# Optimization experiments

Measured on AMD Instinct MI355X. Metric: run time of the kernel, lower is better.

Reference implementation:

```python
import jax, jax.numpy as jnp
import numpy as np
from jax import lax

B, N, C = 8, 8192, 91          # batch, num_boxes, num_classes (incl. background)
CM = C - 1                      # foreground classes
K = 1000                        # pre_nms_num_detections (per-class candidates / max per class)
MAX_TOTAL = 100                 # post_nms_num_detections
IOU_THR = 0.3
SCORE_THR = 0.0
BBOX_W = (10.0, 10.0, 5.0, 5.0)
BBOX_CLIP = float(np.log(1000.0 / 16.0))
IMG = 1024.0


def setup_inputs() -> dict:
    key = jax.random.key(0)
    k1, k2, k3, k4, k5, k6 = jax.random.split(key, 6)
    class_outputs = jax.random.normal(k1, (B, N, C), jnp.float32)
    box_outputs = jax.random.normal(k2, (B, N, C * 4), jnp.float32)
    cy = jax.random.uniform(k3, (B, N), minval=0.0, maxval=IMG)
    cx = jax.random.uniform(k4, (B, N), minval=0.0, maxval=IMG)
    sh = jax.random.uniform(k5, (B, N), minval=16.0, maxval=256.0)
    sw = jax.random.uniform(k6, (B, N), minval=16.0, maxval=256.0)
    anchor_boxes = jnp.stack([
        jnp.clip(cy - 0.5 * sh, 0.0, IMG), jnp.clip(cx - 0.5 * sw, 0.0, IMG),
        jnp.clip(cy + 0.5 * sh, 0.0, IMG), jnp.clip(cx + 0.5 * sw, 0.0, IMG)], axis=-1)
    image_info = jnp.tile(jnp.array([IMG, IMG, 1.0, 1.0], jnp.float32), (B, 1))
    return {"class_outputs": class_outputs, "box_outputs": box_outputs,
            "anchor_boxes": anchor_boxes, "image_info": image_info}


def decode_boxes(enc, anchors):
    # enc, anchors: [..., 4] (ty,tx,th,tw) / (ymin,xmin,ymax,xmax)
    wy, wx, wh, ww = BBOX_W
    ah = anchors[..., 2] - anchors[..., 0]
    aw = anchors[..., 3] - anchors[..., 1]
    acy = anchors[..., 0] + 0.5 * ah
    acx = anchors[..., 1] + 0.5 * aw
    ty = enc[..., 0] / wy
    tx = enc[..., 1] / wx
    th = jnp.minimum(enc[..., 2] / wh, BBOX_CLIP)
    tw = jnp.minimum(enc[..., 3] / ww, BBOX_CLIP)
    cy = ty * ah + acy
    cx = tx * aw + acx
    h = jnp.exp(th) * ah
    w = jnp.exp(tw) * aw
    return jnp.stack([cy - 0.5 * h, cx - 0.5 * w, cy + 0.5 * h, cx + 0.5 * w], axis=-1)


def pairwise_iou(b):  # b: [K,4] -> [K,K]
    area = jnp.maximum(b[:, 2] - b[:, 0], 0.0) * jnp.maximum(b[:, 3] - b[:, 1], 0.0)
    ih = jnp.maximum(jnp.minimum(b[:, None, 2], b[None, :, 2]) - jnp.maximum(b[:, None, 0], b[None, :, 0]), 0.0)
    iw = jnp.maximum(jnp.minimum(b[:, None, 3], b[None, :, 3]) - jnp.maximum(b[:, None, 1], b[None, :, 1]), 0.0)
    inter = ih * iw
    return inter / (area[:, None] + area[None, :] - inter + 1e-8)


def _per_class_nms(bc, sc):
    # bc: [N,4] normalized boxes, sc: [N] scores -> (kept boxes [K,4], scores [K], suppressed -> -1)
    sk, idx = lax.top_k(sc, K)
    bk = bc[idx]
    overlap = pairwise_iou(bk) > IOU_THR   # bool [K,K], sorted by score desc
    pass_thr = sk > SCORE_THR
    def body(i, keep):
        sup = jnp.any(keep & overlap[:, i])
        return keep.at[i].set(pass_thr[i] & jnp.logical_not(sup))
    keep = lax.fori_loop(0, K, body, jnp.zeros((K,), jnp.bool_))
    return bk, jnp.where(keep, sk, -1.0)


def _per_image(norm_boxes, sc):
    # norm_boxes: [N,CM,4], sc: [N,CM]
    bks, sks = jax.vmap(_per_class_nms)(jnp.transpose(norm_boxes, (1, 0, 2)), sc.T)
    fs = sks.reshape(-1)          # [CM*K]
    fb = bks.reshape(-1, 4)
    ts, ti = lax.top_k(fs, MAX_TOTAL)
    tb = fb[ti]
    tc = (ti // K).astype(jnp.float32)   # 0-based fg class index
    valid = ts > SCORE_THR
    ts = jnp.where(valid, ts, 0.0)
    tb = jnp.where(valid[:, None], tb, 0.0)
    tc = jnp.where(valid, tc, 0.0)
    return tb, ts, tc, jnp.sum(valid).astype(jnp.int32)


def reference(class_outputs, box_outputs, anchor_boxes, image_info):
    probs = jax.nn.softmax(class_outputs, axis=-1)
    scores = probs[..., 1:]                                   # [B,N,CM]
    enc = box_outputs.reshape(B, N, C, 4)[:, :, 1:, :]        # [B,N,CM,4]
    anchors = jnp.broadcast_to(anchor_boxes[:, :, None, :], (B, N, CM, 4))
    boxes = decode_boxes(enc, anchors)                        # [B,N,CM,4]
    h = image_info[:, 0]
    w = image_info[:, 1]
    hw = jnp.stack([h, w, h, w], axis=-1)                     # [B,4]
    boxes = jnp.clip(boxes, 0.0, hw[:, None, None, :])        # clip to image
    norm_boxes = boxes / hw[:, None, None, :]                 # to_normalized_coordinates
    pb, ps, pc, nv = lax.map(lambda a: _per_image(*a), (norm_boxes, scores))
    post_boxes = pb * hw[:, None, :]                          # to_absolute_coordinates
    post_classes = pc + 1.0                                   # shift back over background
    return (nv, post_boxes, post_classes, ps)
```

## Files before the change

### kernel.cpp

```cpp
#include <hip/hip_runtime.h>
#include <math.h>

#define Bb 8
#define Nn 8192
#define Cc 91
#define CM 90
#define Kk 1000
#define MAXT 100
#define KSEL 256
#define NW 4
#define IOU_THR 0.3f
#define BBOX_CLIP 4.135166556742356f
#define IMG 1024.0f
#define SM_ROWS 64

typedef unsigned long long u64;
typedef unsigned int u32;

__global__ __launch_bounds__(64) void softmax_scores(
    const float* __restrict__ cls, float* __restrict__ scores_t) {
    __shared__ float rowbuf[SM_ROWS * Cc];
    int blk = blockIdx.x;
    int lane = threadIdx.x;
    const float4* src = (const float4*)(cls + (size_t)blk * SM_ROWS * Cc);
    for (int i = lane; i < SM_ROWS * Cc / 4; i += 64) {
        float4 v = src[i];
        *(float4*)&rowbuf[i * 4] = v;
    }
    __syncthreads();
    int row_g = blk * SM_ROWS + lane;
    int b = row_g >> 13;
    int n = row_g & (Nn - 1);
    float* row = &rowbuf[lane * Cc];
    float m = row[0];
    for (int c = 1; c < Cc; c++) m = fmaxf(m, row[c]);
    float s = 0.0f;
    for (int c = 0; c < Cc; c++) {
        float e = expf(row[c] - m);
        row[c] = e;
        s += e;
    }
    for (int c = 1; c < Cc; c++) {
        float p = row[c] / s;
        scores_t[((size_t)(b * CM + (c - 1))) * Nn + n] = p;
    }
}

__global__ __launch_bounds__(512) void topk_nms(
    const float* __restrict__ scores_t,
    const float* __restrict__ box_out, const float* __restrict__ anchors,
    u64* __restrict__ cand_key, float* __restrict__ cand_box) {
    __shared__ __align__(16) char smem[21264];
    int* hist1 = (int*)smem;
    int* hist2 = (int*)(smem + 4096);
    u64* keys  = (u64*)(smem + 8192);
    int* eqidx = (int*)(smem + 10240);
    u64* keys2 = (u64*)(smem + 11264);
    float* dy1 = (float*)(smem + 13312);
    float* dx1 = (float*)(smem + 14336);
    float* dy2 = (float*)(smem + 15360);
    float* dx2 = (float*)(smem + 16384);
    float* dar = (float*)(smem + 17408);
    float4* kb = (float4*)(smem + 18432);
    float* kar = (float*)(smem + 20032);
    u64* kkey  = (u64*)(smem + 20432);
    int* scal  = (int*)(smem + 21232);
    #define sh_need  scal[0]
    #define sh_digit scal[1]
    #define sh_cnt   scal[2]
    #define sh_eq    scal[3]
    #define sh_kcnt  scal[4]

    int bc = blockIdx.x;
    int b = bc / CM;
    int c = bc % CM;
    int tid = threadIdx.x;
    int wave = tid >> 6, lane = tid & 63;

    hist1[tid] = 0; hist1[tid + 512] = 0;
    hist2[tid] = 0; hist2[tid + 512] = 0;
    if (tid == 0) { sh_need = KSEL; sh_cnt = 0; sh_eq = 0; }
    __syncthreads();

    const float4* s4 = (const float4*)(scores_t + (size_t)bc * Nn);
    float4 v0 = s4[tid];
    float4 v1 = s4[tid + 512];
    float4 v2 = s4[tid + 1024];
    float4 v3 = s4[tid + 1536];
    u32 x[16];
    x[0]  = __float_as_uint(v0.x); x[1]  = __float_as_uint(v0.y);
    x[2]  = __float_as_uint(v0.z); x[3]  = __float_as_uint(v0.w);
    x[4]  = __float_as_uint(v1.x); x[5]  = __float_as_uint(v1.y);
    x[6]  = __float_as_uint(v1.z); x[7]  = __float_as_uint(v1.w);
    x[8]  = __float_as_uint(v2.x); x[9]  = __float_as_uint(v2.y);
    x[10] = __float_as_uint(v2.z); x[11] = __float_as_uint(v2.w);
    x[12] = __float_as_uint(v3.x); x[13] = __float_as_uint(v3.y);
    x[14] = __float_as_uint(v3.z); x[15] = __float_as_uint(v3.w);
    #pragma unroll
    for (int k = 0; k < 16; k++) atomicAdd(&hist1[x[k] >> 20], 1);
    __syncthreads();

    #define SELECT_DIGIT(H)                                                  \
    {                                                                        \
        int4 h0 = *(const int4*)&(H)[16 * lane];                             \
        int4 h1 = *(const int4*)&(H)[16 * lane + 4];                         \
        int4 h2 = *(const int4*)&(H)[16 * lane + 8];                         \
        int4 h3 = *(const int4*)&(H)[16 * lane + 12];                        \
        int cnt[16] = {h0.x, h0.y, h0.z, h0.w, h1.x, h1.y, h1.z, h1.w,       \
                       h2.x, h2.y, h2.z, h2.w, h3.x, h3.y, h3.z, h3.w};      \
        int gsum = 0;                                                        \
        _Pragma("unroll")                                                    \
        for (int j = 0; j < 16; j++) gsum += cnt[j];                         \
        int run = gsum;                                                      \
        for (int off = 1; off < 64; off <<= 1) {                             \
            int vv = __shfl_down(run, off, 64);                              \
            if (lane + off < 64) run += vv;                                  \
        }                                                                    \
        int sa = run - gsum;                                                 \
        int need = sh_need;                                                  \
        if (need > sa && need <= sa + gsum) {                                \
            int acc = sa;                                                    \
            _Pragma("unroll")                                                \
            for (int j = 15; j >= 0; j--) {                                  \
                if (acc + cnt[j] >= need) {                                  \
                    sh_digit = 16 * lane + j;                                \
                    sh_need = need - acc;                                    \
                    break;                                                   \
                }                                                            \
                acc += cnt[j];                                               \
            }                                                                \
        }                                                                    \
    }

    if (wave == 0) SELECT_DIGIT(hist1);
    __syncthreads();
    u32 P12 = (u32)sh_digit;

    #pragma unroll
    for (int k = 0; k < 16; k++)
        if ((x[k] >> 20) == P12) atomicAdd(&hist2[(x[k] >> 10) & 1023], 1);
    __syncthreads();

    if (wave == 0) { SELECT_DIGIT(hist2); }
    else { for (int i = tid - 64; i < 1024; i += 448) hist1[i] = 0; }
    __syncthreads();
    u32 P22 = (P12 << 10) | (u32)sh_digit;

    #pragma unroll
    for (int k = 0; k < 16; k++)
        if ((x[k] >> 10) == P22) atomicAdd(&hist1[x[k] & 1023], 1);
    __syncthreads();

    if (wave == 0) SELECT_DIGIT(hist1);
    __syncthreads();
    u32 Tb = (P22 << 10) | (u32)sh_digit;
    int m = sh_need;
    #undef SELECT_DIGIT

    #pragma unroll
    for (int k = 0; k < 16; k++) {
        u32 v = x[k];
        int idx = ((k >> 2) << 11) + (tid << 2) + (k & 3);
        if (v > Tb) {
            int pp = atomicAdd(&sh_cnt, 1);
            keys[pp] = ((u64)v << 13) | (u64)(8191 - idx);
        } else if (v == Tb) {
            int pp = atomicAdd(&sh_eq, 1);
            if (pp < 256) eqidx[pp] = idx;
        }
    }
    __syncthreads();
    if (tid == 0) {
        int e = min(sh_eq, 256);
        for (int t = 0; t < m; t++) {
            int best = -1, bi = 0x7FFFFFFF;
            for (int q = 0; q < e; q++) {
                int ii = eqidx[q];
                if (ii < bi) { bi = ii; best = q; }
            }
            if (best >= 0) {
                eqidx[best] = 0x7FFFFFFF;
                int pp = atomicAdd(&sh_cnt, 1);
                keys[pp] = ((u64)Tb << 13) | (u64)(8191 - bi);
            }
        }
    }
    __syncthreads();

    if (tid < KSEL) {
        u64 my = keys[tid];
        int n = 8191 - (int)(my & 0x1FFF);
        const float4 e = *(const float4*)(box_out + ((size_t)(b * Nn + n)) * (Cc * 4) + (size_t)(c + 1) * 4);
        const float4 a = *(const float4*)(anchors + (size_t)(b * Nn + n) * 4);
        int r = 0;
        #pragma unroll 8
        for (int q = 0; q < KSEL; q++) r += (keys[q] > my) ? 1 : 0;
        keys2[r] = my;
        float ah = a.z - a.x, aw = a.w - a.y;
        float acy = a.x + 0.5f * ah, acx = a.y + 0.5f * aw;
        float ty = e.x / 10.0f, tx = e.y / 10.0f;
        float th = fminf(e.z / 5.0f, BBOX_CLIP);
        float tw = fminf(e.w / 5.0f, BBOX_CLIP);
        float cy = ty * ah + acy, cx = tx * aw + acx;
        float h = expf(th) * ah, w = expf(tw) * aw;
        float y1 = cy - 0.5f * h, x1 = cx - 0.5f * w;
        float y2 = cy + 0.5f * h, x2 = cx + 0.5f * w;
        y1 = fminf(fmaxf(y1, 0.0f), IMG) * (1.0f / IMG);
        x1 = fminf(fmaxf(x1, 0.0f), IMG) * (1.0f / IMG);
        y2 = fminf(fmaxf(y2, 0.0f), IMG) * (1.0f / IMG);
        x2 = fminf(fmaxf(x2, 0.0f), IMG) * (1.0f / IMG);
        float area = fmaxf(y2 - y1, 0.0f) * fmaxf(x2 - x1, 0.0f);
        dy1[r] = y1; dx1[r] = x1;
        dy2[r] = y2; dx2[r] = x2;
        dar[r] = area;
    }
    __syncthreads();

    if (tid < 64) {
        int kcnt = 0;
        for (int ci = 0; ci < NW && kcnt < MAXT; ci++) {
            int i = ci * 64 + lane;
            u64 key = keys2[i];
            float sc = __uint_as_float((u32)(key >> 13));
            float y1 = dy1[i], x1 = dx1[i];
            float y2 = dy2[i], x2 = dx2[i];
            float area = dar[i];

            bool sup = false;
            for (int r = 0; r < kcnt; r++) {
                float4 kv = kb[r];
                float ka = kar[r];
                float ih = fmaxf(fminf(kv.z, y2) - fmaxf(kv.x, y1), 0.0f);
                float iw = fmaxf(fminf(kv.w, x2) - fmaxf(kv.y, x1), 0.0f);
                float inter = ih * iw;
                sup = sup | (inter > IOU_THR * (ka + area - inter + 1e-8f));
            }
            u64 rem = __ballot((sc > 0.0f) && !sup);
            while (rem != 0ull && kcnt < MAXT) {
                int j = __ffsll(rem) - 1;
                rem &= rem - 1;
                float jy1 = __shfl(y1, j), jx1 = __shfl(x1, j);
                float jy2 = __shfl(y2, j), jx2 = __shfl(x2, j);
                float jar = __shfl(area, j);
                if (lane == j) {
                    kb[kcnt] = make_float4(y1, x1, y2, x2);
                    kar[kcnt] = area;
                    int flat = c * Kk + i;
                    kkey[kcnt] = ((u64)__float_as_uint(sc) << 32)
                               | ((u64)(u32)(131071 - flat) << 14)
                               | (u64)(u32)(c * MAXT + kcnt);
                }
                float ih = fmaxf(fminf(jy2, y2) - fmaxf(jy1, y1), 0.0f);
                float iw = fmaxf(fminf(jx2, x2) - fmaxf(jx1, x1), 0.0f);
                float inter = ih * iw;
                bool ov = inter > IOU_THR * (jar + area - inter + 1e-8f);
                u64 mm = __ballot(ov);
                rem &= ~mm;
                kcnt++;
            }
        }
        if (lane == 0) sh_kcnt = kcnt;
    }
    __syncthreads();

    int kcnt = sh_kcnt;
    for (int r = tid; r < MAXT; r += 512) {
        int slot = bc * MAXT + r;
        if (r < kcnt) {
            cand_key[slot] = kkey[r];
            float4 v = kb[r];
            cand_box[slot * 4 + 0] = v.x;
            cand_box[slot * 4 + 1] = v.y;
            cand_box[slot * 4 + 2] = v.z;
            cand_box[slot * 4 + 3] = v.w;
        } else {
            cand_key[slot] = 0ull;
        }
    }
    #undef sh_need
    #undef sh_digit
    #undef sh_cnt
    #undef sh_eq
    #undef sh_kcnt
}

__global__ __launch_bounds__(256) void final_topk(
    const u64* __restrict__ cand_key, const float* __restrict__ cand_box,
    float* __restrict__ out) {
    extern __shared__ u64 sk[];
    __shared__ u64 res[MAXT];
    int b = blockIdx.x;
    int tid = threadIdx.x;

    for (int i = tid; i < CM * MAXT; i += 256)
        sk[i] = cand_key[b * CM * MAXT + i];
    __syncthreads();

    if (tid < 64) {
        int lane = tid;
        int c0 = lane, c1 = lane + 64;
        bool h1 = c1 < CM;
        int p0 = 0, p1 = 0;
        u64 k0 = sk[c0 * MAXT + 0];
        u64 k0n = sk[c0 * MAXT + 1];
        u64 k1 = h1 ? sk[c1 * MAXT + 0] : 0ull;
        u64 k1n = h1 ? sk[c1 * MAXT + 1] : 0ull;
        for (int t = 0; t < MAXT; t++) {
            u64 m = (k0 > k1) ? k0 : k1;
            for (int off = 32; off > 0; off >>= 1) {
                u64 o = __shfl_xor(m, off);
                if (o > m) m = o;
            }
            if (lane == 0) res[t] = m;
            if (m != 0ull) {
                if (m == k0) {
                    p0++; k0 = k0n;
                    k0n = (p0 + 1 < MAXT) ? sk[c0 * MAXT + p0 + 1] : 0ull;
                } else if (h1 && m == k1) {
                    p1++; k1 = k1n;
                    k1n = (p1 + 1 < MAXT) ? sk[c1 * MAXT + p1 + 1] : 0ull;
                }
            }
        }
    }
    __syncthreads();

    for (int t = tid; t < MAXT; t += 256) {
        u64 m = res[t];
        float sc = __uint_as_float((u32)(m >> 32));
        bool valid = sc > 0.0f;
        float b0 = 0.f, b1 = 0.f, b2 = 0.f, b3 = 0.f, clsv = 0.f, sv = 0.f;
        if (valid) {
            int idx = (int)(m & 0x3FFF);
            int slot = b * CM * MAXT + idx;
            b0 = cand_box[slot * 4 + 0] * IMG;
            b1 = cand_box[slot * 4 + 1] * IMG;
            b2 = cand_box[slot * 4 + 2] * IMG;
            b3 = cand_box[slot * 4 + 3] * IMG;
            clsv = (float)(idx / MAXT + 1);
            sv = sc;
        }
        int o = (b * MAXT + t);
        out[8 + o * 4 + 0] = b0;
        out[8 + o * 4 + 1] = b1;
        out[8 + o * 4 + 2] = b2;
        out[8 + o * 4 + 3] = b3;
        out[8 + Bb * MAXT * 4 + o] = clsv;
        out[8 + Bb * MAXT * 5 + o] = sv;
    }
    if (tid == 0) {
        int nv = 0;
        for (int t = 0; t < MAXT; t++) nv += ((res[t] >> 32) != 0ull) ? 1 : 0;
        out[b] = (float)nv;
    }
}

extern "C" void kernel_launch(void* const* d_in, const int* in_sizes, int n_in,
                              void* d_out, int out_size, void* d_ws, size_t ws_size,
                              hipStream_t stream) {
    (void)in_sizes; (void)n_in; (void)out_size; (void)ws_size;
    const float* cls  = (const float*)d_in[0];
    const float* boxo = (const float*)d_in[1];
    const float* anch = (const float*)d_in[2];
    float* out = (float*)d_out;
    char* ws = (char*)d_ws;

    float* scores_t = (float*)(ws);
    u64*   cand_key = (u64*)  (ws + 23592960);
    float* cand_box = (float*)(ws + 24168960);

    softmax_scores<<<(Bb * Nn) / SM_ROWS, 64, 0, stream>>>(cls, scores_t);
    topk_nms<<<Bb * CM, 512, 0, stream>>>(scores_t, boxo, anch, cand_key, cand_box);
    final_topk<<<Bb, 256, CM * MAXT * sizeof(u64), stream>>>(cand_key, cand_box, out);
}
```

Baseline: 251.9 us.

## Replace serial wave merge in final top-k with radix select plus rank sort

The final per-image top-100 no longer uses a single-wave 100-step merge with shuffle reductions. It now runs a three-pass 10-bit radix histogram select over the score bits of all 9000 candidate keys, gathers the keys above the threshold, fills ties serially, and places each of the 100 survivors by counting its rank. The NMS loop also reads the accepted box's coordinates from shared arrays instead of broadcasting them with shuffles. The aim is to cut the long serial latency of the final merge, at the cost of several more block barriers and shared-memory atomics.

```diff
diff --git a/kernel.cpp b/kernel.cpp
--- a/kernel.cpp
+++ b/kernel.cpp
@@ -155,7 +155,6 @@
     __syncthreads();
     u32 Tb = (P22 << 10) | (u32)sh_digit;
     int m = sh_need;
-    #undef SELECT_DIGIT
 
     #pragma unroll
     for (int k = 0; k < 16; k++) {
@@ -239,9 +238,10 @@
             while (rem != 0ull && kcnt < MAXT) {
                 int j = __ffsll(rem) - 1;
                 rem &= rem - 1;
-                float jy1 = __shfl(y1, j), jx1 = __shfl(x1, j);
-                float jy2 = __shfl(y2, j), jx2 = __shfl(x2, j);
-                float jar = __shfl(area, j);
+                int jg = ci * 64 + j;
+                float jy1 = dy1[jg], jx1 = dx1[jg];
+                float jy2 = dy2[jg], jx2 = dx2[jg];
+                float jar = dar[jg];
                 if (lane == j) {
                     kb[kcnt] = make_float4(y1, x1, y2, x2);
                     kar[kcnt] = area;
@@ -277,6 +277,7 @@
             cand_key[slot] = 0ull;
         }
     }
+    #undef SELECT_DIGIT
     #undef sh_need
     #undef sh_digit
     #undef sh_cnt
@@ -288,50 +289,134 @@
     const u64* __restrict__ cand_key, const float* __restrict__ cand_box,
     float* __restrict__ out) {
     extern __shared__ u64 sk[];
+    __shared__ int hist[1024];
+    __shared__ u64 eqk[512];
+    __shared__ u64 sel[128];
     __shared__ u64 res[MAXT];
+    __shared__ int scal[4];
+    #define sh_need  scal[0]
+    #define sh_digit scal[1]
+    #define sh_cnt   scal[2]
+    #define sh_eq    scal[3]
+
     int b = blockIdx.x;
     int tid = threadIdx.x;
+    int wave = tid >> 6, lane = tid & 63;
 
     for (int i = tid; i < CM * MAXT; i += 256)
         sk[i] = cand_key[b * CM * MAXT + i];
-    __syncthreads();
-
-    if (tid < 64) {
-        int lane = tid;
-        int c0 = lane, c1 = lane + 64;
-        bool h1 = c1 < CM;
-        int p0 = 0, p1 = 0;
-        u64 k0 = sk[c0 * MAXT + 0];
-        u64 k0n = sk[c0 * MAXT + 1];
-        u64 k1 = h1 ? sk[c1 * MAXT + 0] : 0ull;
-        u64 k1n = h1 ? sk[c1 * MAXT + 1] : 0ull;
-        for (int t = 0; t < MAXT; t++) {
-            u64 m = (k0 > k1) ? k0 : k1;
-            for (int off = 32; off > 0; off >>= 1) {
-                u64 o = __shfl_xor(m, off);
-                if (o > m) m = o;
-            }
-            if (lane == 0) res[t] = m;
-            if (m != 0ull) {
-                if (m == k0) {
-                    p0++; k0 = k0n;
-                    k0n = (p0 + 1 < MAXT) ? sk[c0 * MAXT + p0 + 1] : 0ull;
-                } else if (h1 && m == k1) {
-                    p1++; k1 = k1n;
-                    k1n = (p1 + 1 < MAXT) ? sk[c1 * MAXT + p1 + 1] : 0ull;
-                }
-            }
-        }
+    for (int i = tid; i < 1024; i += 256) hist[i] = 0;
+    if (tid == 0) { sh_need = MAXT; sh_cnt = 0; sh_eq = 0; }
+    __syncthreads();
+
+    #define SELECT_DIGIT(H)                                                  \
+    {                                                                        \
+        int4 h0 = *(const int4*)&(H)[16 * lane];                             \
+        int4 h1 = *(const int4*)&(H)[16 * lane + 4];                         \
+        int4 h2 = *(const int4*)&(H)[16 * lane + 8];                         \
+        int4 h3 = *(const int4*)&(H)[16 * lane + 12];                        \
+        int cnt[16] = {h0.x, h0.y, h0.z, h0.w, h1.x, h1.y, h1.z, h1.w,       \
+                       h2.x, h2.y, h2.z, h2.w, h3.x, h3.y, h3.z, h3.w};      \
+        int gsum = 0;                                                        \
+        _Pragma("unroll")                                                    \
+        for (int j = 0; j < 16; j++) gsum += cnt[j];                         \
+        int run = gsum;                                                      \
+        for (int off = 1; off < 64; off <<= 1) {                             \
+            int vv = __shfl_down(run, off, 64);                              \
+            if (lane + off < 64) run += vv;                                  \
+        }                                                                    \
+        int sa = run - gsum;                                                 \
+        int need = sh_need;                                                  \
+        if (need > sa && need <= sa + gsum) {                                \
+            int acc = sa;                                                    \
+            _Pragma("unroll")                                                \
+            for (int j = 15; j >= 0; j--) {                                  \
+                if (acc + cnt[j] >= need) {                                  \
+                    sh_digit = 16 * lane + j;                                \
+                    sh_need = need - acc;                                    \
+                    break;                                                   \
+                }                                                            \
+                acc += cnt[j];                                               \
+            }                                                                \
+        }                                                                    \
+    }
+
+    for (int i = tid; i < CM * MAXT; i += 256) {
+        u32 sb = (u32)(sk[i] >> 32);
+        atomicAdd(&hist[sb >> 20], 1);
+    }
+    __syncthreads();
+    if (wave == 0) SELECT_DIGIT(hist);
+    __syncthreads();
+    u32 P12 = (u32)sh_digit;
+
+    for (int i = tid; i < 1024; i += 256) hist[i] = 0;
+    __syncthreads();
+    for (int i = tid; i < CM * MAXT; i += 256) {
+        u32 sb = (u32)(sk[i] >> 32);
+        if ((sb >> 20) == P12) atomicAdd(&hist[(sb >> 10) & 1023], 1);
+    }
+    __syncthreads();
+    if (wave == 0) SELECT_DIGIT(hist);
+    __syncthreads();
+    u32 P22 = (P12 << 10) | (u32)sh_digit;
+
+    for (int i = tid; i < 1024; i += 256) hist[i] = 0;
+    __syncthreads();
+    for (int i = tid; i < CM * MAXT; i += 256) {
+        u32 sb = (u32)(sk[i] >> 32);
+        if ((sb >> 10) == P22) atomicAdd(&hist[sb & 1023], 1);
+    }
+    __syncthreads();
+    if (wave == 0) SELECT_DIGIT(hist);
+    __syncthreads();
+    u32 Ts = (P22 << 10) | (u32)sh_digit;
+    int m = sh_need;
+    #undef SELECT_DIGIT
+
+    for (int i = tid; i < CM * MAXT; i += 256) {
+        u64 k = sk[i];
+        u32 sb = (u32)(k >> 32);
+        if (sb > Ts) {
+            int pp = atomicAdd(&sh_cnt, 1);
+            sel[pp] = k;
+        } else if (sb == Ts) {
+            int pp = atomicAdd(&sh_eq, 1);
+            if (pp < 512) eqk[pp] = k;
+        }
+    }
+    __syncthreads();
+    if (tid == 0) {
+        int e = min(sh_eq, 512);
+        int base = sh_cnt;
+        for (int t = 0; t < m; t++) {
+            u64 best = 0ull; int bq = -1;
+            for (int q = 0; q < e; q++)
+                if (eqk[q] > best) { best = eqk[q]; bq = q; }
+            if (bq >= 0) eqk[bq] = 0ull;
+            sel[base + t] = best;
+        }
+    }
+    __syncthreads();
+
+    if (tid < MAXT) {
+        u64 my = sel[tid];
+        int r = 0;
+        for (int q = 0; q < MAXT; q++) {
+            u64 o = sel[q];
+            r += (o > my || (o == my && q < tid)) ? 1 : 0;
+        }
+        res[r] = my;
     }
     __syncthreads();
 
     for (int t = tid; t < MAXT; t += 256) {
-        u64 m = res[t];
-        float sc = __uint_as_float((u32)(m >> 32));
+        u64 m2 = res[t];
+        float sc = __uint_as_float((u32)(m2 >> 32));
         bool valid = sc > 0.0f;
         float b0 = 0.f, b1 = 0.f, b2 = 0.f, b3 = 0.f, clsv = 0.f, sv = 0.f;
         if (valid) {
-            int idx = (int)(m & 0x3FFF);
+            int idx = (int)(m2 & 0x3FFF);
             int slot = b * CM * MAXT + idx;
             b0 = cand_box[slot * 4 + 0] * IMG;
             b1 = cand_box[slot * 4 + 1] * IMG;
@@ -353,6 +438,10 @@
         for (int t = 0; t < MAXT; t++) nv += ((res[t] >> 32) != 0ull) ? 1 : 0;
         out[b] = (float)nv;
     }
+    #undef sh_need
+    #undef sh_digit
+    #undef sh_cnt
+    #undef sh_eq
 }
 
 extern "C" void kernel_launch(void* const* d_in, const int* in_sizes, int n_in,
```

Measured after the change: 232.0 us. -7.9%, faster.
